# Kernel optimization log

Hardware: AMD Instinct MI355X
Metric: run time of the kernel (lower is better)

Reference implementation:

```python
import jax, jax.numpy as jnp
import numpy as np

N = 50000   # num_entities
F = 300     # node feature dim
D = 128     # embedding_dim
H = 4       # heads
C = D // H  # per-head out channels (32)
E = 640000  # num edges
R = 200     # num_relations
L = 2       # num_layers
NEG_SLOPE = 0.2  # PyG GATv2Conv default


def setup_inputs() -> dict:
    key = jax.random.key(0)
    ks = jax.random.split(key, 14)
    s = 0.1
    return {
        "entity": jnp.arange(N, dtype=jnp.int32),
        "edge_index": jax.random.randint(ks[0], (2, E), 0, N, dtype=jnp.int32),
        "edge_type": jax.random.randint(ks[1], (E,), 0, R, dtype=jnp.int32),
        # learned parameters
        "node_features": jax.random.normal(ks[2], (N, F), jnp.float32) * s,   # entity_embedding table
        "rel_emb": jax.random.normal(ks[3], (R, D), jnp.float32) * s,          # relation_embedding
        "proj_w": jax.random.normal(ks[4], (F, D), jnp.float32) * s,           # project Linear
        "proj_b": jnp.zeros((D,), jnp.float32),
        # per-layer GATv2Conv params, stacked over L layers
        "w_l": jax.random.normal(ks[5], (L, D, H * C), jnp.float32) * s,       # lin_l weight
        "b_l": jnp.zeros((L, H * C), jnp.float32),
        "w_r": jax.random.normal(ks[6], (L, D, H * C), jnp.float32) * s,       # lin_r weight
        "b_r": jnp.zeros((L, H * C), jnp.float32),
        "w_e": jax.random.normal(ks[7], (L, D, H * C), jnp.float32) * s,       # lin_edge weight (no bias)
        "att": jax.random.normal(ks[8], (L, H, C), jnp.float32) * s,           # attention vector a
        "bias": jnp.zeros((L, H * C), jnp.float32),                             # output bias
    }


def _gatv2_layer(x, src, dst, edge_attr, w_l, b_l, w_r, b_r, w_e, att, bias):
    # x: [N, D], edge_attr: [E, D]
    x_l = (x @ w_l + b_l).reshape(N, H, C)
    x_r = (x @ w_r + b_r).reshape(N, H, C)
    e = (edge_attr @ w_e).reshape(E, H, C)
    # per-edge message (gather src/dst + edge), GATv2: leaky_relu BEFORE attention dot
    m = jax.nn.leaky_relu(x_l[src] + x_r[dst] + e, NEG_SLOPE)   # [E, H, C]
    logits = jnp.einsum('ehc,hc->eh', m, att)                    # [E, H]
    # segment softmax over edges grouped by destination node
    lmax = jax.ops.segment_max(logits, dst, num_segments=N)      # [N, H]
    ex = jnp.exp(logits - lmax[dst])                             # [E, H]
    denom = jax.ops.segment_sum(ex, dst, num_segments=N)         # [N, H]
    alpha = ex / denom[dst]                                      # [E, H]
    # scatter-aggregate messages x_l[src] weighted by alpha
    out = jax.ops.segment_sum(x_l[src] * alpha[:, :, None], dst, num_segments=N)  # [N, H, C]
    return out.reshape(N, H * C) + bias


def reference(entity, edge_index, edge_type, node_features, rel_emb,
              proj_w, proj_b, w_l, b_l, w_r, b_r, w_e, att, bias):
    x = node_features[entity]            # embedding lookup
    x = x @ proj_w + proj_b              # project to D
    edge_attr = rel_emb[edge_type]       # [E, D] (weights=False -> no edge_weight scaling)
    src, dst = edge_index[0], edge_index[1]
    for i in range(L):
        x = _gatv2_layer(x, src, dst, edge_attr,
                         w_l[i], b_l[i], w_r[i], b_r[i], w_e[i], att[i], bias[i])
        if i != L - 1:
            x = jax.nn.elu(x)            # dropout inactive (eval mode)
    return x
```

## Files before the change

### kernel.cpp

```cpp
#include <hip/hip_runtime.h>

#define NN 50000
#define FF 300
#define DD 128
#define HH 4
#define CC 32
#define EE 640000
#define RR 200
#define LL 2
#define SB ((NN + 255) / 256)
#define PK 320
#define WCONV (2 * 128 * 128)
#define WTOT (2 * 128 * PK + WCONV)
#define HB ((EE + 255) / 256)
#define WB (WCONV / 256)
#define FB PK
#define RB (LL * RR / 2)

typedef unsigned short u16;
typedef unsigned int u32;
typedef _Float16 h2   __attribute__((ext_vector_type(2)));
typedef _Float16 half8 __attribute__((ext_vector_type(8)));
typedef __attribute__((ext_vector_type(4))) float floatx4;
typedef u32 u32x4 __attribute__((ext_vector_type(4)));

__device__ __forceinline__ u16 f2h(float f) {
    union { _Float16 h; u16 u; } v; v.h = (_Float16)f; return v.u;
}
__device__ __forceinline__ float h2f(u16 u) {
    union { u16 u; _Float16 h; } v; v.u = u; return (float)v.h;
}
__device__ __forceinline__ h2 u2h2(u32 p) {
    union { u32 u; h2 h; } v; v.u = p; return v.h;
}
__device__ __forceinline__ h2 hmax2(h2 a, h2 b) {
#if __has_builtin(__builtin_elementwise_max)
    return __builtin_elementwise_max(a, b);
#else
    h2 r; r.x = a.x > b.x ? a.x : b.x; r.y = a.y > b.y ? a.y : b.y; return r;
#endif
}
__device__ __forceinline__ float hdot2(h2 a, h2 b, float c) {
#if __has_builtin(__builtin_amdgcn_fdot2)
    return __builtin_amdgcn_fdot2(a, b, c, false);
#else
    return c + (float)a.x * (float)b.x + (float)a.y * (float)b.y;
#endif
}

__device__ __forceinline__ int block_excl_scan(int v, int* lds4, int* total) {
    int lane = threadIdx.x & 63, wid = threadIdx.x >> 6;
    int x = v;
    #pragma unroll
    for (int off = 1; off < 64; off <<= 1) {
        int y = __shfl_up(x, off, 64);
        if (lane >= off) x += y;
    }
    if (lane == 63) lds4[wid] = x;
    __syncthreads();
    int add = 0;
    #pragma unroll
    for (int w = 0; w < 4; w++) add += (w < wid) ? lds4[w] : 0;
    *total = lds4[0] + lds4[1] + lds4[2] + lds4[3];
    return x + add - v;
}

__global__ __launch_bounds__(256)
void prep_kernel(const int* __restrict__ ei, int* __restrict__ counts,
                 const float* __restrict__ proj_w, const float* __restrict__ w_l,
                 const float* __restrict__ w_r, u16* __restrict__ wt,
                 const float* __restrict__ rel_emb, const float* __restrict__ w_e,
                 u16* __restrict__ erel, const float* __restrict__ proj_b,
                 const float* __restrict__ b_l, const float* __restrict__ b_r,
                 float* __restrict__ fbias)
{
    __shared__ float rv[2][DD];
    int b = blockIdx.x, tid = threadIdx.x;
    if (b < HB) {
        int e = b * 256 + tid;
        if (e < EE) atomicAdd(&counts[ei[EE + e]], 1);
    } else if (b < HB + WB) {
        int i = (b - HB) * 256 + tid;
        int seg = i >> 14;
        int r = i & 16383;
        int n = r >> 7, k = r & 127;
        const float* src = (seg == 0 ? w_l : w_r) + (size_t)DD * DD;
        wt[2 * 128 * PK + i] = f2h(src[(size_t)k * DD + n]);
    } else if (b < HB + WB + FB) {
        int half = tid >> 7, d = tid & 127;
        int pp = (b - HB - WB) * 2 + half;
        int lr = pp / PK, k = pp - lr * PK;
        rv[half][d] = (k < FF) ? proj_w[(size_t)k * DD + d] : 0.f;
        __syncthreads();
        float acc = 0.f;
        if (k < FF) {
            const float* W = lr ? w_r : w_l;
            #pragma unroll 8
            for (int j = 0; j < DD; j++) acc += rv[half][j] * W[(size_t)j * DD + d];
        }
        wt[(size_t)lr * 128 * PK + (size_t)d * PK + k] = f2h(acc);
    } else if (b == HB + WB + FB) {
        int half = tid >> 7, d = tid & 127;
        if (tid < DD) rv[0][tid] = proj_b[tid];
        __syncthreads();
        const float* W = half ? w_r : w_l;
        float acc = half ? b_r[d] : b_l[d];
        #pragma unroll 8
        for (int j = 0; j < DD; j++) acc += rv[0][j] * W[(size_t)j * DD + d];
        fbias[half * DD + d] = acc;
    } else {
        int half = tid >> 7, d = tid & 127;
        int lr = (b - HB - WB - FB - 1) * 2 + half;
        int l = lr / RR, r = lr - l * RR;
        rv[half][d] = rel_emb[r * DD + d];
        __syncthreads();
        const float* W = w_e + (size_t)l * DD * DD;
        float acc = 0.f;
        #pragma unroll 8
        for (int k = 0; k < DD; k++) acc += rv[half][k] * W[k * DD + d];
        erel[(size_t)lr * DD + d] = f2h(acc);
    }
}

template<bool AF16, bool GATHER, int K>
__global__ __launch_bounds__(256)
void gemm_stage1_kernel(const void* __restrict__ A_, const int* __restrict__ rowidx,
                        int lda, int Ka,
                        const u16* __restrict__ BT1, const float* __restrict__ bias1,
                        u16* __restrict__ C1,
                        const u16* __restrict__ BT2, const float* __restrict__ bias2,
                        u16* __restrict__ C2, int M)
{
    __shared__ u16 As[64][K + 8];
    int tid  = threadIdx.x;
    int m0   = blockIdx.x * 64;
    int wave = tid >> 6, lane = tid & 63;
    int quad = lane >> 4, l16 = lane & 15;
    const u16* BT = (wave < 2) ? BT1 : BT2;
    int wcol = (wave & 1) * 64;

    floatx4 acc[4][4];
    #pragma unroll
    for (int i = 0; i < 4; i++)
        #pragma unroll
        for (int j = 0; j < 4; j++) acc[i][j] = (floatx4){0.f, 0.f, 0.f, 0.f};

    const u16* Brow[4];
    #pragma unroll
    for (int j = 0; j < 4; j++) Brow[j] = BT + (size_t)(wcol + j * 16 + l16) * K;

    int ar = tid >> 2, ac = (tid & 3) * 16;
    int arow = m0 + ar;
    int rid = (arow < M) ? (GATHER ? rowidx[arow] : arow) : 0;

    #pragma unroll
    for (int c = 0; c < K / 64; c++) {
        int kb = c * 64 + ac;
        u16 tmp[16];
        if (AF16) {
            const u16* Ap = (const u16*)A_ + (size_t)rid * lda + kb;
            *(half8*)&tmp[0] = *(const half8*)Ap;
            *(half8*)&tmp[8] = *(const half8*)(Ap + 8);
        } else {
            const float* Ap = (const float*)A_ + (size_t)rid * lda + kb;
            if (kb + 16 <= Ka) {
                #pragma unroll
                for (int qq = 0; qq < 4; qq++) {
                    float4 f = *(const float4*)(Ap + qq * 4);
                    tmp[qq*4+0] = f2h(f.x); tmp[qq*4+1] = f2h(f.y);
                    tmp[qq*4+2] = f2h(f.z); tmp[qq*4+3] = f2h(f.w);
                }
            } else {
                #pragma unroll
                for (int j = 0; j < 16; j++) tmp[j] = (kb + j < Ka) ? f2h(Ap[j]) : (u16)0;
            }
        }
        *(half8*)&As[ar][kb]     = *(half8*)&tmp[0];
        *(half8*)&As[ar][kb + 8] = *(half8*)&tmp[8];
    }
    __syncthreads();

    #pragma unroll
    for (int kk = 0; kk < K; kk += 32) {
        half8 af[4], bf[4];
        #pragma unroll
        for (int j = 0; j < 4; j++)
            bf[j] = *(const half8*)(Brow[j] + kk + quad * 8);
        #pragma unroll
        for (int i = 0; i < 4; i++)
            af[i] = *(const half8*)&As[i * 16 + l16][kk + quad * 8];
        #pragma unroll
        for (int i = 0; i < 4; i++)
            #pragma unroll
            for (int j = 0; j < 4; j++)
                acc[i][j] = __builtin_amdgcn_mfma_f32_16x16x32_f16(
                    af[i], bf[j], acc[i][j], 0, 0, 0);
    }

    u16* Cw = (wave < 2) ? C1 : C2;
    const float* bw = (wave < 2) ? bias1 : bias2;
    #pragma unroll
    for (int i = 0; i < 4; i++) {
        #pragma unroll
        for (int rr = 0; rr < 4; rr++) {
            int row = m0 + i * 16 + quad * 4 + rr;
            if (row < M) {
                #pragma unroll
                for (int j = 0; j < 4; j++) {
                    int col = wcol + j * 16 + l16;
                    Cw[(size_t)row * DD + col] = f2h(acc[i][j][rr] + bw[col]);
                }
            }
        }
    }
}

__global__ __launch_bounds__(256)
void scan_local_kernel(const int* __restrict__ counts, int* __restrict__ offsets,
                       int* __restrict__ bsum)
{
    __shared__ int lds4[4];
    int i = blockIdx.x * 256 + threadIdx.x;
    int v = (i < NN) ? counts[i] : 0;
    int total;
    int ex = block_excl_scan(v, lds4, &total);
    if (i < NN) offsets[i] = ex;
    if (threadIdx.x == 0) bsum[blockIdx.x] = total;
}

__global__ __launch_bounds__(256)
void scan_bsum_kernel(int* __restrict__ bsum)
{
    __shared__ int lds4[4];
    int t = threadIdx.x;
    int v = (t < SB) ? bsum[t] : 0;
    int total;
    int ex = block_excl_scan(v, lds4, &total);
    if (t < SB) bsum[t] = ex;
}

__global__ __launch_bounds__(256)
void scatter_kernel(const int* __restrict__ ei, const int* __restrict__ et,
                    const int* __restrict__ offsets, const int* __restrict__ bsum,
                    int* __restrict__ fill, u32* __restrict__ dstorder)
{
    int e = blockIdx.x * 256 + threadIdx.x;
    if (e >= EE) return;
    int d = ei[EE + e];
    int pos = offsets[d] + bsum[d >> 8] + atomicAdd(&fill[d], 1);
    dstorder[pos] = (u32)ei[e] | ((u32)et[e] << 16);
}

__global__ __launch_bounds__(256)
void node_kernel(const u32* __restrict__ dstorder, const int* __restrict__ offsets,
                 const int* __restrict__ bsum,
                 const u16* __restrict__ xl, const u16* __restrict__ xr,
                 const u16* __restrict__ erel, const float* __restrict__ att,
                 const float* __restrict__ bias,
                 u16* __restrict__ xnext, float* __restrict__ outp, int is_last)
{
    int tid  = threadIdx.x;
    int node = blockIdx.x * 4 + (tid >> 6);
    int lane = tid & 63;
    if (node >= NN) return;
    int g  = lane >> 4;
    int gl = lane & 15;
    int c0 = gl * 8;
    int beg = offsets[node] + bsum[node >> 8];
    int end = (node == NN - 1) ? EE : offsets[node + 1] + bsum[(node + 1) >> 8];

    h2 xrh[4], atth[4];
    {
        u32x4 xrv = *(const u32x4*)&xr[(size_t)node * DD + c0];
        #pragma unroll
        for (int q = 0; q < 4; q++) xrh[q] = u2h2(xrv[q]);
        #pragma unroll
        for (int q = 0; q < 4; q++) {
            float2 av = *(const float2*)&att[c0 + q * 2];
            atth[q] = (h2){(_Float16)av.x, (_Float16)av.y};
        }
    }
    const h2 c02 = (h2){(_Float16)0.2f, (_Float16)0.2f};

    float s = 0.f;
    h2 a2[4];
    #pragma unroll
    for (int q = 0; q < 4; q++) a2[q] = (h2){(_Float16)0.f, (_Float16)0.f};

    for (int base = beg; base < end; base += 4) {
        int es = base + g;
        bool valid = es < end;
        u32 st = valid ? dstorder[es] : 0;
        int src = st & 0xffff;
        int typ = st >> 16;
        u32x4 xv = *(const u32x4*)&xl[(size_t)src * DD + c0];
        u32x4 ev = *(const u32x4*)&erel[(size_t)typ * DD + c0];
        h2 xh[4];
        float p = 0.f;
        #pragma unroll
        for (int q = 0; q < 4; q++) {
            xh[q] = u2h2(xv[q]);
            h2 m = (xh[q] + xrh[q]) + u2h2(ev[q]);
            m = hmax2(m, m * c02);
            p = hdot2(m, atth[q], p);
        }
        p += __shfl_xor(p, 1, 64);
        p += __shfl_xor(p, 2, 64);
        float w = valid ? __expf(fminf(p, 60.f)) : 0.f;
        s += w;
        h2 wh = (h2){(_Float16)w, (_Float16)w};
        #pragma unroll
        for (int q = 0; q < 4; q++) a2[q] += wh * xh[q];
    }

    float a[8];
    #pragma unroll
    for (int q = 0; q < 4; q++) { a[q*2] = (float)a2[q].x; a[q*2+1] = (float)a2[q].y; }
    #pragma unroll
    for (int j = 0; j < 8; j++) {
        a[j] += __shfl_xor(a[j], 16, 64);
        a[j] += __shfl_xor(a[j], 32, 64);
    }
    s += __shfl_xor(s, 16, 64);
    s += __shfl_xor(s, 32, 64);

    if (lane < 16) {
        float rh = 1.f / fmaxf(s, 1e-30f);
        float4 b0 = *(const float4*)&bias[c0];
        float4 b1 = *(const float4*)&bias[c0 + 4];
        float bv[8] = {b0.x, b0.y, b0.z, b0.w, b1.x, b1.y, b1.z, b1.w};
        float v[8];
        #pragma unroll
        for (int j = 0; j < 8; j++) v[j] = a[j] * rh + bv[j];
        if (is_last) {
            float4* op = (float4*)&outp[(size_t)node * DD + c0];
            op[0] = make_float4(v[0], v[1], v[2], v[3]);
            op[1] = make_float4(v[4], v[5], v[6], v[7]);
        } else {
            u16 pk[8];
            #pragma unroll
            for (int j = 0; j < 8; j++) {
                float w2 = v[j] > 0.f ? v[j] : __expf(v[j]) - 1.f;
                pk[j] = f2h(w2);
            }
            *(half8*)&xnext[(size_t)node * DD + c0] = *(half8*)pk;
        }
    }
}

extern "C" void kernel_launch(void* const* d_in, const int* in_sizes, int n_in,
                              void* d_out, int out_size, void* d_ws, size_t ws_size,
                              hipStream_t stream)
{
    const int*   entity        = (const int*)d_in[0];
    const int*   edge_index    = (const int*)d_in[1];
    const int*   edge_type     = (const int*)d_in[2];
    const float* node_features = (const float*)d_in[3];
    const float* rel_emb       = (const float*)d_in[4];
    const float* proj_w        = (const float*)d_in[5];
    const float* proj_b        = (const float*)d_in[6];
    const float* w_l           = (const float*)d_in[7];
    const float* b_l           = (const float*)d_in[8];
    const float* w_r           = (const float*)d_in[9];
    const float* b_r           = (const float*)d_in[10];
    const float* w_e           = (const float*)d_in[11];
    const float* att           = (const float*)d_in[12];
    const float* bias          = (const float*)d_in[13];

    u16*   xb      = (u16*)d_ws;
    u16*   xl      = xb + (size_t)NN * DD;
    u16*   xr      = xl + (size_t)NN * DD;
    u16*   erel    = xr + (size_t)NN * DD;
    u16*   wt      = erel + (size_t)LL * RR * DD;
    u32*   dstorder= (u32*)(wt + WTOT);
    int*   counts  = (int*)(dstorder + (size_t)EE);
    int*   fill    = counts + NN;
    int*   offsets = fill + NN;
    int*   bsum    = offsets + NN;
    float* fbias   = (float*)(bsum + SB);

    hipMemsetAsync(counts, 0, (size_t)NN * 2 * sizeof(int), stream);
    prep_kernel<<<HB + WB + FB + 1 + RB, 256, 0, stream>>>(
        edge_index, counts, proj_w, w_l, w_r, wt, rel_emb, w_e, erel,
        proj_b, b_l, b_r, fbias);

    scan_local_kernel<<<SB, 256, 0, stream>>>(counts, offsets, bsum);
    scan_bsum_kernel<<<1, 256, 0, stream>>>(bsum);
    scatter_kernel<<<(EE + 255) / 256, 256, 0, stream>>>(
        edge_index, edge_type, offsets, bsum, fill, dstorder);

    const int GB2 = (NN + 63) / 64;

    gemm_stage1_kernel<false, true, PK><<<GB2, 256, 0, stream>>>(
        node_features, entity, FF, FF,
        wt, fbias, xl,
        wt + (size_t)128 * PK, fbias + DD, xr, NN);
    node_kernel<<<(NN + 3) / 4, 256, 0, stream>>>(
        dstorder, offsets, bsum, xl, xr, erel,
        att, bias, xb, (float*)d_out, 0);

    gemm_stage1_kernel<true, false, DD><<<GB2, 256, 0, stream>>>(
        xb, nullptr, DD, DD,
        wt + (size_t)2 * 128 * PK, b_l + DD, xl,
        wt + (size_t)2 * 128 * PK + 128 * 128, b_r + DD, xr, NN);
    node_kernel<<<(NN + 3) / 4, 256, 0, stream>>>(
        dstorder, offsets, bsum, xl, xr, erel + (size_t)RR * DD,
        att + DD, bias + DD, xb, (float*)d_out, 1);
}
```

Baseline: 327.1 us.

## Use 8-wave GEMM blocks with B-fragment prefetch and 32-bit gather offsets

```diff
diff --git a/kernel.cpp b/kernel.cpp
--- a/kernel.cpp
+++ b/kernel.cpp
@@ -123,82 +123,85 @@
 }
 
 template<bool AF16, bool GATHER, int K>
-__global__ __launch_bounds__(256)
-void gemm_stage1_kernel(const void* __restrict__ A_, const int* __restrict__ rowidx,
-                        int lda, int Ka,
-                        const u16* __restrict__ BT1, const float* __restrict__ bias1,
-                        u16* __restrict__ C1,
-                        const u16* __restrict__ BT2, const float* __restrict__ bias2,
-                        u16* __restrict__ C2, int M)
+__global__ __launch_bounds__(512)
+void gemm8_kernel(const void* __restrict__ A_, const int* __restrict__ rowidx,
+                  int lda, int Ka,
+                  const u16* __restrict__ BT1, const float* __restrict__ bias1,
+                  u16* __restrict__ C1,
+                  const u16* __restrict__ BT2, const float* __restrict__ bias2,
+                  u16* __restrict__ C2, int M)
 {
     __shared__ u16 As[64][K + 8];
     int tid  = threadIdx.x;
     int m0   = blockIdx.x * 64;
     int wave = tid >> 6, lane = tid & 63;
     int quad = lane >> 4, l16 = lane & 15;
-    const u16* BT = (wave < 2) ? BT1 : BT2;
-    int wcol = (wave & 1) * 64;
-
-    floatx4 acc[4][4];
+    const u16* BT = (wave < 4) ? BT1 : BT2;
+    int wcol = (wave & 3) * 32;
+
+    floatx4 acc[4][2];
     #pragma unroll
     for (int i = 0; i < 4; i++)
         #pragma unroll
-        for (int j = 0; j < 4; j++) acc[i][j] = (floatx4){0.f, 0.f, 0.f, 0.f};
-
-    const u16* Brow[4];
-    #pragma unroll
-    for (int j = 0; j < 4; j++) Brow[j] = BT + (size_t)(wcol + j * 16 + l16) * K;
-
-    int ar = tid >> 2, ac = (tid & 3) * 16;
+        for (int j = 0; j < 2; j++) acc[i][j] = (floatx4){0.f, 0.f, 0.f, 0.f};
+
+    const u16* Brow[2];
+    #pragma unroll
+    for (int j = 0; j < 2; j++) Brow[j] = BT + (size_t)(wcol + j * 16 + l16) * K;
+
+    half8 bfc[2];
+    #pragma unroll
+    for (int j = 0; j < 2; j++) bfc[j] = *(const half8*)(Brow[j] + quad * 8);
+
+    int ar = tid >> 3, at = tid & 7;
     int arow = m0 + ar;
     int rid = (arow < M) ? (GATHER ? rowidx[arow] : arow) : 0;
-
     #pragma unroll
     for (int c = 0; c < K / 64; c++) {
-        int kb = c * 64 + ac;
-        u16 tmp[16];
+        int kb = c * 64 + at * 8;
+        u16 tmp[8];
         if (AF16) {
             const u16* Ap = (const u16*)A_ + (size_t)rid * lda + kb;
-            *(half8*)&tmp[0] = *(const half8*)Ap;
-            *(half8*)&tmp[8] = *(const half8*)(Ap + 8);
+            *(half8*)tmp = *(const half8*)Ap;
         } else {
             const float* Ap = (const float*)A_ + (size_t)rid * lda + kb;
-            if (kb + 16 <= Ka) {
-                #pragma unroll
-                for (int qq = 0; qq < 4; qq++) {
-                    float4 f = *(const float4*)(Ap + qq * 4);
-                    tmp[qq*4+0] = f2h(f.x); tmp[qq*4+1] = f2h(f.y);
-                    tmp[qq*4+2] = f2h(f.z); tmp[qq*4+3] = f2h(f.w);
-                }
+            if (kb + 8 <= Ka) {
+                float4 f0 = *(const float4*)Ap;
+                float4 f1 = *(const float4*)(Ap + 4);
+                tmp[0] = f2h(f0.x); tmp[1] = f2h(f0.y); tmp[2] = f2h(f0.z); tmp[3] = f2h(f0.w);
+                tmp[4] = f2h(f1.x); tmp[5] = f2h(f1.y); tmp[6] = f2h(f1.z); tmp[7] = f2h(f1.w);
             } else {
                 #pragma unroll
-                for (int j = 0; j < 16; j++) tmp[j] = (kb + j < Ka) ? f2h(Ap[j]) : (u16)0;
+                for (int jj = 0; jj < 8; jj++) tmp[jj] = (kb + jj < Ka) ? f2h(Ap[jj]) : (u16)0;
             }
         }
-        *(half8*)&As[ar][kb]     = *(half8*)&tmp[0];
-        *(half8*)&As[ar][kb + 8] = *(half8*)&tmp[8];
+        *(half8*)&As[ar][kb] = *(half8*)tmp;
     }
     __syncthreads();
 
     #pragma unroll
     for (int kk = 0; kk < K; kk += 32) {
-        half8 af[4], bf[4];
-        #pragma unroll
-        for (int j = 0; j < 4; j++)
-            bf[j] = *(const half8*)(Brow[j] + kk + quad * 8);
+        half8 bfn[2];
+        if (kk + 32 < K) {
+            #pragma unroll
+            for (int j = 0; j < 2; j++)
+                bfn[j] = *(const half8*)(Brow[j] + kk + 32 + quad * 8);
+        }
+        half8 af[4];
         #pragma unroll
         for (int i = 0; i < 4; i++)
             af[i] = *(const half8*)&As[i * 16 + l16][kk + quad * 8];
         #pragma unroll
         for (int i = 0; i < 4; i++)
             #pragma unroll
-            for (int j = 0; j < 4; j++)
+            for (int j = 0; j < 2; j++)
                 acc[i][j] = __builtin_amdgcn_mfma_f32_16x16x32_f16(
-                    af[i], bf[j], acc[i][j], 0, 0, 0);
-    }
-
-    u16* Cw = (wave < 2) ? C1 : C2;
-    const float* bw = (wave < 2) ? bias1 : bias2;
+                    af[i], bfc[j], acc[i][j], 0, 0, 0);
+        bfc[0] = bfn[0]; bfc[1] = bfn[1];
+    }
+
+    u16* Cw = (wave < 4) ? C1 : C2;
+    const float* bw = (wave < 4) ? bias1 : bias2;
     #pragma unroll
     for (int i = 0; i < 4; i++) {
         #pragma unroll
@@ -206,7 +209,7 @@
             int row = m0 + i * 16 + quad * 4 + rr;
             if (row < M) {
                 #pragma unroll
-                for (int j = 0; j < 4; j++) {
+                for (int j = 0; j < 2; j++) {
                     int col = wcol + j * 16 + l16;
                     Cw[(size_t)row * DD + col] = f2h(acc[i][j][rr] + bw[col]);
                 }
@@ -271,7 +274,7 @@
 
     h2 xrh[4], atth[4];
     {
-        u32x4 xrv = *(const u32x4*)&xr[(size_t)node * DD + c0];
+        u32x4 xrv = *(const u32x4*)(xr + ((u32)node * DD + c0));
         #pragma unroll
         for (int q = 0; q < 4; q++) xrh[q] = u2h2(xrv[q]);
         #pragma unroll
@@ -291,10 +294,10 @@
         int es = base + g;
         bool valid = es < end;
         u32 st = valid ? dstorder[es] : 0;
-        int src = st & 0xffff;
-        int typ = st >> 16;
-        u32x4 xv = *(const u32x4*)&xl[(size_t)src * DD + c0];
-        u32x4 ev = *(const u32x4*)&erel[(size_t)typ * DD + c0];
+        u32 xoff = (st & 0xffffu) * DD + (u32)c0;
+        u32 eoff = (st >> 16) * DD + (u32)c0;
+        u32x4 xv = *(const u32x4*)(xl + xoff);
+        u32x4 ev = *(const u32x4*)(erel + eoff);
         h2 xh[4];
         float p = 0.f;
         #pragma unroll
@@ -333,7 +336,7 @@
         #pragma unroll
         for (int j = 0; j < 8; j++) v[j] = a[j] * rh + bv[j];
         if (is_last) {
-            float4* op = (float4*)&outp[(size_t)node * DD + c0];
+            float4* op = (float4*)(outp + ((u32)node * DD + c0));
             op[0] = make_float4(v[0], v[1], v[2], v[3]);
             op[1] = make_float4(v[4], v[5], v[6], v[7]);
         } else {
@@ -343,7 +346,7 @@
                 float w2 = v[j] > 0.f ? v[j] : __expf(v[j]) - 1.f;
                 pk[j] = f2h(w2);
             }
-            *(half8*)&xnext[(size_t)node * DD + c0] = *(half8*)pk;
+            *(half8*)(xnext + ((u32)node * DD + c0)) = *(half8*)pk;
         }
     }
 }
@@ -391,7 +394,7 @@
 
     const int GB2 = (NN + 63) / 64;
 
-    gemm_stage1_kernel<false, true, PK><<<GB2, 256, 0, stream>>>(
+    gemm8_kernel<false, true, PK><<<GB2, 512, 0, stream>>>(
         node_features, entity, FF, FF,
         wt, fbias, xl,
         wt + (size_t)128 * PK, fbias + DD, xr, NN);
@@ -399,7 +402,7 @@
         dstorder, offsets, bsum, xl, xr, erel,
         att, bias, xb, (float*)d_out, 0);
 
-    gemm_stage1_kernel<true, false, DD><<<GB2, 256, 0, stream>>>(
+    gemm8_kernel<true, false, DD><<<GB2, 512, 0, stream>>>(
         xb, nullptr, DD, DD,
         wt + (size_t)2 * 128 * PK, b_l + DD, xl,
         wt + (size_t)2 * 128 * PK + 128 * 128, b_r + DD, xr, NN);
```

Measured after the change: 325.0 us. About the same (-0.6%).
